# Optimization experiments

Hardware: AMD Instinct MI355X
Metric: run time of the kernel (lower is better)

The kernel has to match this reference:

```python
import jax, jax.numpy as jnp
import numpy as np


def setup_inputs() -> dict:
    key = jax.random.key(0)
    k1, k2, k3 = jax.random.split(key, 3)
    B, D = 4096, 784
    O1, O2 = 8192, 8192
    x = jax.random.normal(k1, (B, D), dtype=jnp.float32)
    idx1 = jax.random.randint(k2, (O1, 2), 0, D, dtype=jnp.int32)
    idx2 = jax.random.randint(k3, (O2, 3), 0, D, dtype=jnp.int32)
    return {"x": x, "idx1": idx1, "idx2": idx2}


def _order_terms(x, idx):
    # x: (B, D), idx: (O, order) -> (B, O)
    # gather x[:, idx] -> (B, O, order), product over the order axis
    gathered = x[:, idx]
    return jnp.prod(gathered, axis=-1)


def reference(x, idx1, idx2):
    out1 = _order_terms(x, idx1)  # (B, O1)
    out2 = _order_terms(x, idx2)  # (B, O2)
    return jnp.concatenate([out1, out2], axis=-1)  # (B, O1+O2)
```

## Files before the change

kernel.cpp:

```cpp
#include <hip/hip_runtime.h>
#include <hip/hip_bf16.h>

constexpr int B  = 4096;
constexpr int D  = 784;
constexpr int O1 = 8192;
constexpr int O2 = 8192;
constexpr int OT = O1 + O2;

constexpr int TPB  = 256;
constexpr int ROWS = 4;
constexpr int VEC  = 4;
constexpr int COLS = TPB * VEC;

__global__ __launch_bounds__(TPB) void randomde_kernel(
    const float* __restrict__ x,
    const int*   __restrict__ idx1,
    const int*   __restrict__ idx2,
    float*       __restrict__ out)
{
    __shared__ float xs[ROWS][D];

    const int colChunk = blockIdx.x;
    const int rowChunk = blockIdx.y;
    const int row0     = rowChunk * ROWS;
    const int tid      = threadIdx.x;

    {
        const float4* __restrict__ x4 = (const float4*)(x + (size_t)row0 * D);
        float4* xs4 = (float4*)&xs[0][0];
        constexpr int N4 = ROWS * (D / 4);
        #pragma unroll
        for (int i = tid; i < N4; i += TPB) {
            xs4[i] = x4[i];
        }
    }
    __syncthreads();

    const int colBase = colChunk * COLS + tid * VEC;

    float res[ROWS][VEC];

    if (colBase < O1) {
        #pragma unroll
        for (int v = 0; v < VEC; ++v) {
            const int c  = colBase + v;
            const int a  = idx1[c * 2 + 0];
            const int b_ = idx1[c * 2 + 1];
            #pragma unroll
            for (int r = 0; r < ROWS; ++r) {
                res[r][v] = xs[r][a] * xs[r][b_];
            }
        }
    } else {
        #pragma unroll
        for (int v = 0; v < VEC; ++v) {
            const int c  = colBase - O1 + v;
            const int a  = idx2[c * 3 + 0];
            const int b_ = idx2[c * 3 + 1];
            const int e  = idx2[c * 3 + 2];
            #pragma unroll
            for (int r = 0; r < ROWS; ++r) {
                res[r][v] = xs[r][a] * xs[r][b_] * xs[r][e];
            }
        }
    }

    #pragma unroll
    for (int r = 0; r < ROWS; ++r) {
        float4 val = make_float4(res[r][0], res[r][1], res[r][2], res[r][3]);
        *(float4*)(out + (size_t)(row0 + r) * OT + colBase) = val;
    }
}

extern "C" void kernel_launch(void* const* d_in, const int* in_sizes, int n_in,
                              void* d_out, int out_size, void* d_ws, size_t ws_size,
                              hipStream_t stream) {
    const float* x    = (const float*)d_in[0];
    const int*   idx1 = (const int*)d_in[1];
    const int*   idx2 = (const int*)d_in[2];
    float*       out  = (float*)d_out;

    dim3 grid(OT / COLS, B / ROWS);
    dim3 block(TPB);
    randomde_kernel<<<grid, block, 0, stream>>>(x, idx1, idx2, out);
}
```

Before: 307.4 us.

## Remap threads to row-by-column tiles with padded LDS and vectorized index loads

Each block now stages 16 rows of x in LDS instead of 4, using a padded row stride of 785 to avoid bank conflicts. Threads are remapped so the 16 lanes of a column group cover the 16 rows and share the same index loads, which are now read as int4 vectors. Each block loops over 2048 output columns. The aim is to reuse index fetches across more rows and cut LDS bank conflicts. The costs are about 50KB of LDS per block, which lowers occupancy, and float4 output stores where only 4 lanes per row write contiguously (64B), which coalesces less well.

```diff
diff --git a/kernel.cpp b/kernel.cpp
--- a/kernel.cpp
+++ b/kernel.cpp
@@ -7,10 +7,13 @@
 constexpr int O2 = 8192;
 constexpr int OT = O1 + O2;
 
-constexpr int TPB  = 256;
-constexpr int ROWS = 4;
-constexpr int VEC  = 4;
-constexpr int COLS = TPB * VEC;
+constexpr int TPB   = 256;
+constexpr int ROWS  = 16;
+constexpr int LDSTR = 785;
+constexpr int CTS   = TPB / ROWS;
+constexpr int VEC   = 4;
+constexpr int CPB   = 2048;
+constexpr int GROUPS = CPB / (CTS * VEC);
 
 __global__ __launch_bounds__(TPB) void randomde_kernel(
     const float* __restrict__ x,
@@ -18,57 +21,54 @@
     const int*   __restrict__ idx2,
     float*       __restrict__ out)
 {
-    __shared__ float xs[ROWS][D];
+    __shared__ float xs[ROWS * LDSTR];
 
-    const int colChunk = blockIdx.x;
-    const int rowChunk = blockIdx.y;
-    const int row0     = rowChunk * ROWS;
-    const int tid      = threadIdx.x;
+    const int tid     = threadIdx.x;
+    const int r       = tid & (ROWS - 1);
+    const int ct      = tid >> 4;
+    const int row0    = blockIdx.y * ROWS;
+    const int colBase = blockIdx.x * CPB;
 
-    {
-        const float4* __restrict__ x4 = (const float4*)(x + (size_t)row0 * D);
-        float4* xs4 = (float4*)&xs[0][0];
-        constexpr int N4 = ROWS * (D / 4);
+    for (int rr = 0; rr < ROWS; ++rr) {
+        const float* __restrict__ src = x + (size_t)(row0 + rr) * D;
         #pragma unroll
-        for (int i = tid; i < N4; i += TPB) {
-            xs4[i] = x4[i];
+        for (int c = tid; c < D; c += TPB) {
+            xs[rr * LDSTR + c] = src[c];
         }
     }
     __syncthreads();
 
-    const int colBase = colChunk * COLS + tid * VEC;
-
-    float res[ROWS][VEC];
+    const float* __restrict__ xrow = &xs[r * LDSTR];
+    float* __restrict__ outrow = out + (size_t)(row0 + r) * OT;
 
     if (colBase < O1) {
-        #pragma unroll
-        for (int v = 0; v < VEC; ++v) {
-            const int c  = colBase + v;
-            const int a  = idx1[c * 2 + 0];
-            const int b_ = idx1[c * 2 + 1];
-            #pragma unroll
-            for (int r = 0; r < ROWS; ++r) {
-                res[r][v] = xs[r][a] * xs[r][b_];
-            }
+        for (int g = 0; g < GROUPS; ++g) {
+            const int c = colBase + g * (CTS * VEC) + ct * VEC;
+            const int4* __restrict__ p = (const int4*)(idx1 + (size_t)c * 2);
+            const int4 i0 = p[0];
+            const int4 i1 = p[1];
+            float4 v;
+            v.x = xrow[i0.x] * xrow[i0.y];
+            v.y = xrow[i0.z] * xrow[i0.w];
+            v.z = xrow[i1.x] * xrow[i1.y];
+            v.w = xrow[i1.z] * xrow[i1.w];
+            *(float4*)(outrow + c) = v;
         }
     } else {
-        #pragma unroll
-        for (int v = 0; v < VEC; ++v) {
-            const int c  = colBase - O1 + v;
-            const int a  = idx2[c * 3 + 0];
-            const int b_ = idx2[c * 3 + 1];
-            const int e  = idx2[c * 3 + 2];
-            #pragma unroll
-            for (int r = 0; r < ROWS; ++r) {
-                res[r][v] = xs[r][a] * xs[r][b_] * xs[r][e];
-            }
+        for (int g = 0; g < GROUPS; ++g) {
+            const int c  = colBase + g * (CTS * VEC) + ct * VEC;
+            const int c2 = c - O1;
+            const int4* __restrict__ p = (const int4*)(idx2 + (size_t)c2 * 3);
+            const int4 i0 = p[0];
+            const int4 i1 = p[1];
+            const int4 i2 = p[2];
+            float4 v;
+            v.x = xrow[i0.x] * xrow[i0.y] * xrow[i0.z];
+            v.y = xrow[i0.w] * xrow[i1.x] * xrow[i1.y];
+            v.z = xrow[i1.z] * xrow[i1.w] * xrow[i2.x];
+            v.w = xrow[i2.y] * xrow[i2.z] * xrow[i2.w];
+            *(float4*)(outrow + c) = v;
         }
-    }
-
-    #pragma unroll
-    for (int r = 0; r < ROWS; ++r) {
-        float4 val = make_float4(res[r][0], res[r][1], res[r][2], res[r][3]);
-        *(float4*)(out + (size_t)(row0 + r) * OT + colBase) = val;
     }
 }
 
@@ -80,7 +80,7 @@
     const int*   idx2 = (const int*)d_in[2];
     float*       out  = (float*)d_out;
 
-    dim3 grid(OT / COLS, B / ROWS);
+    dim3 grid(OT / CPB, B / ROWS);
     dim3 block(TPB);
     randomde_kernel<<<grid, block, 0, stream>>>(x, idx1, idx2, out);
 }
```

Measured after the change: 418.6 us. +36.2%, slower.
